# Kernel optimization log

Measured on AMD Instinct MI355X. Metric: run time of the kernel, lower is better.

Reference implementation:

```python
import jax, jax.numpy as jnp
import numpy as np

EPS = 1e-07
DEGREE = 3
INPUT_DIM = 256
OUTPUT_DIM = 256
BATCH = 2048


def setup_inputs() -> dict:
    key = jax.random.key(0)
    kx, kc = jax.random.split(key)
    x = jax.random.normal(kx, (BATCH, INPUT_DIM), dtype=jnp.float32)
    std = 1.0 / (INPUT_DIM * (DEGREE + 1))
    cheby_coeffs = jax.random.normal(kc, (INPUT_DIM, OUTPUT_DIM, DEGREE + 1), dtype=jnp.float32) * std
    return {"x": x, "cheby_coeffs": cheby_coeffs}


def reference(x, cheby_coeffs):
    # x: [b, i]; cheby_coeffs: [i, o, d+1]
    input_dim = x.shape[1]
    degree_p1 = cheby_coeffs.shape[2]
    arange = jnp.arange(degree_p1, dtype=x.dtype)  # [d+1]
    t = jnp.tanh(x)
    theta = jnp.arccos(jnp.clip(t, -1.0 + EPS, 1.0 - EPS))  # [b, i]
    basis = jnp.cos(theta[:, :, None] * arange)  # [b, i, d+1] Chebyshev T_k
    # Fused contraction: einsum 'bid,iod->bio' followed by sum over i == 'bid,iod->bo'
    y = jnp.einsum('bid,iod->bo', basis, cheby_coeffs) / input_dim
    return y
```

## Files before the change

### kernel.cpp

```cpp
#include <hip/hip_runtime.h>
#include <hip/hip_bf16.h>
#include <stdint.h>

#define I_DIM   256
#define O_DIM   256
#define NCH     4

typedef float f32x4 __attribute__((ext_vector_type(4)));
typedef short bf16x8 __attribute__((ext_vector_type(8)));

__device__ __forceinline__ uint32_t pk2(float a, float b) {
    __hip_bfloat162 h = __float22bfloat162_rn(make_float2(a, b));
    uint32_t u;
    __builtin_memcpy(&u, &h, 4);
    return u;
}

__device__ __forceinline__ void basis2(float v, uint32_t& lo, uint32_t& hi) {
    float e = __expf(2.0f * v);
    float t = 1.0f - 2.0f / (e + 1.0f);
    float t2 = __builtin_fmaf(2.0f * t, t, -1.0f);
    float t3 = __builtin_fmaf(2.0f * t, t2, -t);
    lo = pk2(1.0f, t);
    hi = pk2(t2, t3);
}

__global__ __launch_bounds__(256, 2) void cheby_mfma(
        const float* __restrict__ x, const float* __restrict__ cc,
        float* __restrict__ out) {
    __shared__ __align__(16) unsigned char lds[65536];

    const int tid  = threadIdx.x;
    const int lane = tid & 63;
    const int wid  = tid >> 6;
    const int bm   = blockIdx.x >> 3;
    const int bn   = blockIdx.x & 7;
    const int m0   = bm * 32;
    const int n0   = bn * 32;

    const int arow = tid >> 3;
    const int aiq  = tid & 7;
    const int bcl  = tid & 31;
    const int big  = tid >> 5;

    const float4* __restrict__ x4 = reinterpret_cast<const float4*>(x);
    const float4* __restrict__ c4 = reinterpret_cast<const float4*>(cc);

    float4 ax0[2], ax1[2], cb[2][8];

    auto loadAB = [&](int ch, int s) {
        const float4* p = &x4[(m0 + arow) * (I_DIM / 4) + ch * 16 + aiq * 2];
        ax0[s] = p[0]; ax1[s] = p[1];
        #pragma unroll
        for (int j = 0; j < 8; ++j)
            cb[s][j] = c4[(ch * 64 + big * 8 + j) * O_DIM + n0 + bcl];
    };

    auto stageAB = [&](int s) {
        const uint32_t abase = (uint32_t)(s * 16384 + arow * 512 + aiq * 64);
        const uint32_t axr   = (uint32_t)((arow & 31) << 4);
        uint32_t w0, w1, w2, w3, w4, w5, w6, w7;
        basis2(ax0[s].x, w0, w1); basis2(ax0[s].y, w2, w3);
        basis2(ax0[s].z, w4, w5); basis2(ax0[s].w, w6, w7);
        *reinterpret_cast<uint4*>(lds + ((abase     ) ^ axr)) = make_uint4(w0, w1, w2, w3);
        *reinterpret_cast<uint4*>(lds + ((abase + 16) ^ axr)) = make_uint4(w4, w5, w6, w7);
        basis2(ax1[s].x, w0, w1); basis2(ax1[s].y, w2, w3);
        basis2(ax1[s].z, w4, w5); basis2(ax1[s].w, w6, w7);
        *reinterpret_cast<uint4*>(lds + ((abase + 32) ^ axr)) = make_uint4(w0, w1, w2, w3);
        *reinterpret_cast<uint4*>(lds + ((abase + 48) ^ axr)) = make_uint4(w4, w5, w6, w7);
        const uint32_t bbase = (uint32_t)(32768 + s * 16384 + bcl * 512 + big * 64);
        const uint32_t bxr   = (uint32_t)((bcl & 31) << 4);
        #pragma unroll
        for (int j = 0; j < 8; j += 2) {
            uint32_t u0 = pk2(cb[s][j].x,     cb[s][j].y);
            uint32_t u1 = pk2(cb[s][j].z,     cb[s][j].w);
            uint32_t u2 = pk2(cb[s][j + 1].x, cb[s][j + 1].y);
            uint32_t u3 = pk2(cb[s][j + 1].z, cb[s][j + 1].w);
            *reinterpret_cast<uint4*>(lds + ((bbase + j * 8) ^ bxr)) = make_uint4(u0, u1, u2, u3);
        }
    };

    const int wr = wid >> 1, wc = wid & 1;
    const int mrow  = wr * 16 + (lane & 15);
    const int bcol  = wc * 16 + (lane & 15);
    const int klane = (lane >> 4) << 3;
    const uint32_t aswz = (uint32_t)((mrow & 31) << 4);
    const uint32_t bswz = (uint32_t)((bcol & 31) << 4);

    f32x4 acc0 = {0.f, 0.f, 0.f, 0.f};
    f32x4 acc1 = {0.f, 0.f, 0.f, 0.f};

    loadAB(0, 0);
    #pragma unroll
    for (int ch = 0; ch < NCH; ++ch) {
        const int s = ch & 1;
        if (ch + 1 < NCH) loadAB(ch + 1, s ^ 1);
        stageAB(s);
        __syncthreads();
        const uint32_t abase = (uint32_t)(s * 16384 + mrow * 512);
        const uint32_t bbase = (uint32_t)(32768 + s * 16384 + bcol * 512);
        __builtin_amdgcn_s_setprio(1);
        #pragma unroll
        for (int ks = 0; ks < 8; ++ks) {
            const uint32_t kb = (uint32_t)((ks * 32 + klane) * 2);
            bf16x8 a = *reinterpret_cast<const bf16x8*>(lds + ((abase + kb) ^ aswz));
            bf16x8 b = *reinterpret_cast<const bf16x8*>(lds + ((bbase + kb) ^ bswz));
            if (ks & 1) acc1 = __builtin_amdgcn_mfma_f32_16x16x32_bf16(a, b, acc1, 0, 0, 0);
            else        acc0 = __builtin_amdgcn_mfma_f32_16x16x32_bf16(a, b, acc0, 0, 0, 0);
        }
        __builtin_amdgcn_s_setprio(0);
    }

    const float sc = 1.0f / 256.0f;
    f32x4 r = acc0 + acc1;
    const int gr = m0 + wr * 16 + ((lane >> 4) << 2);
    const int gc = n0 + wc * 16 + (lane & 15);
    #pragma unroll
    for (int q = 0; q < 4; ++q)
        out[(gr + q) * O_DIM + gc] = r[q] * sc;
}

extern "C" void kernel_launch(void* const* d_in, const int* in_sizes, int n_in,
                              void* d_out, int out_size, void* d_ws, size_t ws_size,
                              hipStream_t stream) {
    (void)in_sizes; (void)n_in; (void)out_size; (void)d_ws; (void)ws_size;
    const float* x  = (const float*)d_in[0];
    const float* cc = (const float*)d_in[1];
    float* out = (float*)d_out;
    cheby_mfma<<<dim3(512), dim3(256), 0, stream>>>(x, cc, out);
}
```

Before: 12.75 us.

## Retile to 16x64 output blocks with smaller K chunks and higher occupancy

Changes the block tile from 32x32 to 16x64 outputs, halves the K chunk per pipeline stage (8 chunks of 32 inputs instead of 4 of 64), and shrinks LDS from 64KB to 40KB so four blocks per CU can be resident. Each wave now covers one 16-column slice of the 64 columns with a shared 16-row A tile. The aim is more latency hiding through occupancy and a shorter per-stage staging cost. In exchange the basis for each x row is recomputed across only 4 column blocks instead of 8, but coefficients are re-read by 128 row blocks instead of 64, and there are more barriers per block.

```diff
diff --git a/kernel.cpp b/kernel.cpp
--- a/kernel.cpp
+++ b/kernel.cpp
@@ -4,7 +4,7 @@
 
 #define I_DIM   256
 #define O_DIM   256
-#define NCH     4
+#define NCH     8
 
 typedef float f32x4 __attribute__((ext_vector_type(4)));
 typedef short bf16x8 __attribute__((ext_vector_type(8)));
@@ -25,51 +25,46 @@
     hi = pk2(t2, t3);
 }
 
-__global__ __launch_bounds__(256, 2) void cheby_mfma(
+__global__ __launch_bounds__(256, 4) void cheby_mfma(
         const float* __restrict__ x, const float* __restrict__ cc,
         float* __restrict__ out) {
-    __shared__ __align__(16) unsigned char lds[65536];
+    __shared__ __align__(16) unsigned char lds[40960];
 
     const int tid  = threadIdx.x;
     const int lane = tid & 63;
     const int wid  = tid >> 6;
-    const int bm   = blockIdx.x >> 3;
-    const int bn   = blockIdx.x & 7;
-    const int m0   = bm * 32;
-    const int n0   = bn * 32;
+    const int bm   = blockIdx.x >> 2;
+    const int bn   = blockIdx.x & 3;
+    const int m0   = bm * 16;
+    const int n0   = bn * 64;
 
-    const int arow = tid >> 3;
-    const int aiq  = tid & 7;
-    const int bcl  = tid & 31;
-    const int big  = tid >> 5;
+    const int arow = tid >> 4;
+    const int apos = tid & 15;
+    const int bcl  = tid & 63;
+    const int big  = tid >> 6;
 
-    const float4* __restrict__ x4 = reinterpret_cast<const float4*>(x);
+    const float2* __restrict__ x2 = reinterpret_cast<const float2*>(x);
     const float4* __restrict__ c4 = reinterpret_cast<const float4*>(cc);
 
-    float4 ax0[2], ax1[2], cb[2][8];
+    float2 ax[2];
+    float4 cb[2][8];
 
     auto loadAB = [&](int ch, int s) {
-        const float4* p = &x4[(m0 + arow) * (I_DIM / 4) + ch * 16 + aiq * 2];
-        ax0[s] = p[0]; ax1[s] = p[1];
+        ax[s] = x2[(m0 + arow) * (I_DIM / 2) + ch * 16 + apos];
         #pragma unroll
         for (int j = 0; j < 8; ++j)
-            cb[s][j] = c4[(ch * 64 + big * 8 + j) * O_DIM + n0 + bcl];
+            cb[s][j] = c4[(ch * 32 + big * 8 + j) * O_DIM + n0 + bcl];
     };
 
     auto stageAB = [&](int s) {
-        const uint32_t abase = (uint32_t)(s * 16384 + arow * 512 + aiq * 64);
-        const uint32_t axr   = (uint32_t)((arow & 31) << 4);
-        uint32_t w0, w1, w2, w3, w4, w5, w6, w7;
-        basis2(ax0[s].x, w0, w1); basis2(ax0[s].y, w2, w3);
-        basis2(ax0[s].z, w4, w5); basis2(ax0[s].w, w6, w7);
-        *reinterpret_cast<uint4*>(lds + ((abase     ) ^ axr)) = make_uint4(w0, w1, w2, w3);
-        *reinterpret_cast<uint4*>(lds + ((abase + 16) ^ axr)) = make_uint4(w4, w5, w6, w7);
-        basis2(ax1[s].x, w0, w1); basis2(ax1[s].y, w2, w3);
-        basis2(ax1[s].z, w4, w5); basis2(ax1[s].w, w6, w7);
-        *reinterpret_cast<uint4*>(lds + ((abase + 32) ^ axr)) = make_uint4(w0, w1, w2, w3);
-        *reinterpret_cast<uint4*>(lds + ((abase + 48) ^ axr)) = make_uint4(w4, w5, w6, w7);
-        const uint32_t bbase = (uint32_t)(32768 + s * 16384 + bcl * 512 + big * 64);
-        const uint32_t bxr   = (uint32_t)((bcl & 31) << 4);
+        const uint32_t abase = (uint32_t)(s * 4096 + arow * 256 + apos * 16);
+        const uint32_t axr   = (uint32_t)((arow & 15) << 4);
+        uint32_t w0, w1, w2, w3;
+        basis2(ax[s].x, w0, w1);
+        basis2(ax[s].y, w2, w3);
+        *reinterpret_cast<uint4*>(lds + (abase ^ axr)) = make_uint4(w0, w1, w2, w3);
+        const uint32_t bbase = (uint32_t)(8192 + s * 16384 + bcl * 256 + big * 64);
+        const uint32_t bxr   = (uint32_t)((bcl & 15) << 4);
         #pragma unroll
         for (int j = 0; j < 8; j += 2) {
             uint32_t u0 = pk2(cb[s][j].x,     cb[s][j].y);
@@ -80,12 +75,11 @@
         }
     };
 
-    const int wr = wid >> 1, wc = wid & 1;
-    const int mrow  = wr * 16 + (lane & 15);
-    const int bcol  = wc * 16 + (lane & 15);
+    const int mrow  = lane & 15;
+    const int bcol  = wid * 16 + (lane & 15);
     const int klane = (lane >> 4) << 3;
-    const uint32_t aswz = (uint32_t)((mrow & 31) << 4);
-    const uint32_t bswz = (uint32_t)((bcol & 31) << 4);
+    const uint32_t aswz = (uint32_t)((mrow & 15) << 4);
+    const uint32_t bswz = (uint32_t)((bcol & 15) << 4);
 
     f32x4 acc0 = {0.f, 0.f, 0.f, 0.f};
     f32x4 acc1 = {0.f, 0.f, 0.f, 0.f};
@@ -97,11 +91,11 @@
         if (ch + 1 < NCH) loadAB(ch + 1, s ^ 1);
         stageAB(s);
         __syncthreads();
-        const uint32_t abase = (uint32_t)(s * 16384 + mrow * 512);
-        const uint32_t bbase = (uint32_t)(32768 + s * 16384 + bcol * 512);
+        const uint32_t abase = (uint32_t)(s * 4096 + mrow * 256);
+        const uint32_t bbase = (uint32_t)(8192 + s * 16384 + bcol * 256);
         __builtin_amdgcn_s_setprio(1);
         #pragma unroll
-        for (int ks = 0; ks < 8; ++ks) {
+        for (int ks = 0; ks < 4; ++ks) {
             const uint32_t kb = (uint32_t)((ks * 32 + klane) * 2);
             bf16x8 a = *reinterpret_cast<const bf16x8*>(lds + ((abase + kb) ^ aswz));
             bf16x8 b = *reinterpret_cast<const bf16x8*>(lds + ((bbase + kb) ^ bswz));
@@ -113,8 +107,8 @@
 
     const float sc = 1.0f / 256.0f;
     f32x4 r = acc0 + acc1;
-    const int gr = m0 + wr * 16 + ((lane >> 4) << 2);
-    const int gc = n0 + wc * 16 + (lane & 15);
+    const int gr = m0 + ((lane >> 4) << 2);
+    const int gc = n0 + wid * 16 + (lane & 15);
     #pragma unroll
     for (int q = 0; q < 4; ++q)
         out[(gr + q) * O_DIM + gc] = r[q] * sc;
```

Result: slower. 13.36 us (+4.8%).
